# Optimization experiments

Measured on AMD Instinct MI355X. Metric: run time of the kernel, lower is better.

Reference implementation:

```python
import jax, jax.numpy as jnp
import numpy as np

# E8P 12-bit-abs codebook construction (faithful vectorized port of the torch code)
_SHUF = np.array([0, 2, 1, 3, 4, 6, 5, 7])  # shuffle_map
# get_norm12() * 2 (the integer matrix before the /2)
_NORM12_X2 = np.array([
    [3, 1, 1, 1, 3, 3, 3, 3], [1, 3, 1, 1, 3, 3, 3, 3], [1, 1, 3, 1, 3, 3, 3, 3],
    [1, 1, 1, 3, 3, 3, 3, 3], [3, 3, 3, 1, 3, 3, 1, 1], [3, 3, 3, 1, 3, 1, 3, 1],
    [3, 3, 3, 1, 1, 3, 3, 1], [3, 3, 3, 1, 3, 1, 1, 3], [3, 3, 3, 1, 1, 3, 1, 3],
    [3, 3, 3, 1, 1, 1, 3, 3], [3, 3, 1, 3, 3, 3, 1, 1], [3, 3, 1, 3, 3, 1, 3, 1],
    [3, 3, 1, 3, 1, 3, 3, 1], [3, 3, 1, 3, 3, 1, 1, 3], [3, 3, 1, 3, 1, 3, 1, 3],
    [3, 3, 1, 3, 1, 1, 3, 3], [3, 1, 3, 3, 3, 3, 1, 1], [3, 1, 3, 3, 3, 1, 3, 1],
    [3, 1, 3, 3, 1, 3, 3, 1], [3, 1, 3, 3, 3, 1, 1, 3], [3, 1, 3, 3, 1, 3, 1, 3],
    [1, 3, 3, 3, 1, 1, 3, 3], [1, 3, 3, 3, 3, 3, 1, 1], [1, 3, 3, 3, 3, 1, 3, 1],
    [1, 3, 3, 3, 1, 3, 3, 1], [1, 3, 3, 3, 3, 1, 1, 3], [1, 3, 3, 3, 1, 3, 1, 3],
    [1, 1, 3, 3, 1, 3, 3, 3], [3, 3, 1, 1, 3, 3, 3, 1]], dtype=np.int64)


def _packed_abs_grid():
    # Enumerate D8+1/2 lattice points, working with doubled integer coords (odd ints in [-7,7])
    idx = np.arange(8 ** 8, dtype=np.int64)
    cols, s, nrm = [], 0, 0
    for i in range(8):  # torch.cartesian_prod order: first dim varies slowest
        v = (2 * (((idx >> (3 * (7 - i))) & 7) - 4) + 1).astype(np.int8)  # 2*x for x in {-3.5..3.5}
        cols.append(v)
        w = v.astype(np.int32)
        s = s + w
        nrm = nrm + w * w
    mask = (s % 4 == 0) & (nrm <= 40)
    V = np.stack([c[mask] for c in cols], axis=1)
    d8abs2 = np.unique(np.abs(V), axis=0).astype(np.int64)  # lexsorted, doubled abs values
    cba2 = np.concatenate([d8abs2, _NORM12_X2], axis=0)[:, _SHUF]  # doubled values (== 2*cba)
    parity = (cba2.sum(1) // 2) % 2  # == cba.sum(1) % 2
    col = cba2 * 2  # == cba * 4, integer byte values in [2,14]
    col[:, 7] = col[:, 7] * (1 - 2 * parity)
    acc = np.zeros(col.shape[0], dtype=np.int64)
    for i in range(8):
        acc = acc | (col[:, i] << (8 * i))
    assert acc.shape[0] == 256
    return acc


def _full_grid():
    # Decode all 2^16 codes into the [65536, 8] fp32 codebook (port of get_full_grid)
    acc = _packed_abs_grid()
    c = np.arange(1 << 16, dtype=np.int64)
    signs = c & 255
    p = signs ^ (signs >> 4)
    p ^= p >> 2
    p ^= p >> 1
    parity = p & 1  # xor of the 8 sign bits
    signs = signs ^ parity
    ac = acc[c >> 8]  # packed abs code per entry
    byt = ((ac[:, None] >> (8 * _SHUF)) & 255).astype(np.uint8).astype(np.int8).astype(np.float32) / 4.0
    neg = ((signs[:, None] >> (7 - _SHUF)) & 1).astype(bool)
    vals = np.where(neg, -byt, byt) + np.where(parity[:, None] == 1, np.float32(-0.25), np.float32(0.25))
    return vals.astype(np.float32)


def setup_inputs() -> dict:
    key = jax.random.key(0)
    k1, k2 = jax.random.split(key)
    B = 4096          # tokens (batch * seq)
    M = 4096          # out_features = Qidxs rows
    N = 512           # Qidxs cols; in_features = N * 8 = 4096
    inp = jax.random.normal(k1, (B, N * 8), dtype=jnp.float32)
    Qidxs = jax.random.randint(k2, (M, N), 0, 1 << 16, dtype=jnp.int32)
    grid = jnp.asarray(_full_grid())  # [65536, 8] fp32 decoded E8P codebook
    return {"input": inp, "Qidxs": Qidxs, "grid": grid}


def reference(input, Qidxs, grid):
    m, n = Qidxs.shape
    # Dequantize: each int16 code indexes an 8-vector of the E8P codebook
    W = jnp.take(grid, Qidxs, axis=0).reshape(m, n * 8)  # [m, n*8] decompressed weight
    return input @ W.T  # [B, m]
```

## Files before the change

kernel.cpp:

```cpp
#include <hip/hip_runtime.h>
#include <hip/hip_bf16.h>

#define B_DIM 4096
#define M_DIM 4096
#define K_DIM 4096
#define NCODE 512

typedef __attribute__((ext_vector_type(4))) float f32x4;
typedef __attribute__((ext_vector_type(8))) short short8;

__device__ __forceinline__ unsigned short f2bf(float f) {
    union { float f; unsigned u; } c; c.f = f;
    unsigned u = c.u;
    return (unsigned short)((u + 0x7FFFu + ((u >> 16) & 1u)) >> 16);
}

__global__ __launch_bounds__(256) void prep_kernel(const int* __restrict__ Q,
                                                   const float* __restrict__ cb,
                                                   short* __restrict__ Wout,
                                                   const float* __restrict__ in,
                                                   short* __restrict__ Ab) {
    const int b = blockIdx.x;
    if (b < 8192) {
        const int t = b * 256 + threadIdx.x;
        const int code = Q[t] & 0xFFFF;
        const float4* g = (const float4*)(cb + (size_t)code * 8);
        const float4 v0 = g[0];
        const float4 v1 = g[1];
        short8 o;
        o[0] = f2bf(v0.x); o[1] = f2bf(v0.y); o[2] = f2bf(v0.z); o[3] = f2bf(v0.w);
        o[4] = f2bf(v1.x); o[5] = f2bf(v1.y); o[6] = f2bf(v1.z); o[7] = f2bf(v1.w);
        *(short8*)(Wout + (size_t)t * 8) = o;
    } else {
        const int t = (b - 8192) * 256 + threadIdx.x;
        const float4* p = (const float4*)(in + (size_t)t * 8);
        const float4 v0 = p[0];
        const float4 v1 = p[1];
        short8 o;
        o[0] = f2bf(v0.x); o[1] = f2bf(v0.y); o[2] = f2bf(v0.z); o[3] = f2bf(v0.w);
        o[4] = f2bf(v1.x); o[5] = f2bf(v1.y); o[6] = f2bf(v1.z); o[7] = f2bf(v1.w);
        *(short8*)(Ab + (size_t)t * 8) = o;
    }
}

#define BM 256
#define BN 256
#define BK 32
#define NT (K_DIM / BK)

#define GLD(src, dst) \
    __builtin_amdgcn_global_load_lds( \
        (const __attribute__((address_space(1))) void*)(src), \
        (__attribute__((address_space(3))) void*)(dst), 16, 0, 0)

#define MFMA(a, b, c) __builtin_amdgcn_mfma_f32_16x16x32_bf16(a, b, c, 0, 0, 0)

__global__ __launch_bounds__(512, 2) void gemm_bt_kernel(const short* __restrict__ A,
                                                         const short* __restrict__ Wd,
                                                         float* __restrict__ C) {
    __shared__ short lds[4 * 16384];

    const int tid  = threadIdx.x;
    const int wave = tid >> 6;
    const int lane = tid & 63;

    const int bid = blockIdx.x;
    const int xcd = bid & 7;
    const int s   = bid >> 3;
    const int by  = (xcd >> 1) * 4 + (s >> 3);
    const int bx  = (xcd & 1) * 8 + (s & 7);

    const int rowBase = by * BM;
    const int colBase = bx * BN;

    const int wr = wave >> 2;
    const int wc = wave & 3;

    const int rA0 = tid >> 2;
    const int uu  = (tid & 3) ^ ((rA0 >> 1) & 3);
    const short* aSrc0 = A  + (size_t)(rowBase + rA0) * K_DIM + uu * 8;
    const short* aSrc1 = A  + (size_t)(rowBase + rA0 + 128) * K_DIM + uu * 8;
    const short* bSrc0 = Wd + (size_t)(colBase + rA0) * K_DIM + uu * 8;
    const short* bSrc1 = Wd + (size_t)(colBase + rA0 + 128) * K_DIM + uu * 8;

    const int l15 = lane & 15;
    const int l4  = lane >> 4;
    const int sx  = (l15 >> 1) & 3;
    const int aRd = (wr * 128 + l15) * 32 + (l4 ^ sx) * 8;
    const int bRd = 8192 + (wc * 64 + l15) * 32 + (l4 ^ sx) * 8;

    f32x4 acc[8][4] = {};

#pragma unroll
    for (int p = 0; p < 3; ++p) {
        const int koff = p * BK;
        short* base = &lds[p * 16384];
        GLD(aSrc0 + koff, base + wave * 512);
        GLD(aSrc1 + koff, base + 4096 + wave * 512);
        GLD(bSrc0 + koff, base + 8192 + wave * 512);
        GLD(bSrc1 + koff, base + 12288 + wave * 512);
    }
    asm volatile("s_waitcnt vmcnt(8)" ::: "memory");
    __builtin_amdgcn_s_barrier();

    for (int t = 0; t < NT; ++t) {
        const int buf    = (t & 3) * 16384;
        const int tpre   = (t + 3 < NT) ? (t + 3) : (NT - 1);
        const int kpre   = tpre * BK;
        const int bufpre = ((t + 3) & 3) * 16384;

        short8 a0[4], b0[4];
#pragma unroll
        for (int m = 0; m < 4; ++m)
            a0[m] = *(const short8*)&lds[buf + aRd + m * 512];
#pragma unroll
        for (int n = 0; n < 4; ++n)
            b0[n] = *(const short8*)&lds[buf + bRd + n * 512];
        GLD(aSrc0 + kpre, &lds[bufpre + wave * 512]);
        GLD(aSrc1 + kpre, &lds[bufpre + 4096 + wave * 512]);
        asm volatile("s_waitcnt vmcnt(6)" ::: "memory");
        __builtin_amdgcn_s_barrier();
        asm volatile("s_waitcnt lgkmcnt(0)" ::: "memory");
        __builtin_amdgcn_sched_barrier(0);
        __builtin_amdgcn_s_setprio(1);
#pragma unroll
        for (int m = 0; m < 4; ++m)
#pragma unroll
            for (int n = 0; n < 4; ++n)
                acc[m][n] = MFMA(a0[m], b0[n], acc[m][n]);
        __builtin_amdgcn_s_setprio(0);
        __builtin_amdgcn_s_barrier();

        short8 a1[4];
#pragma unroll
        for (int m = 0; m < 4; ++m)
            a1[m] = *(const short8*)&lds[buf + aRd + (m + 4) * 512];
        GLD(bSrc0 + kpre, &lds[bufpre + 8192 + wave * 512]);
        GLD(bSrc1 + kpre, &lds[bufpre + 12288 + wave * 512]);
        __builtin_amdgcn_s_barrier();
        asm volatile("s_waitcnt lgkmcnt(0)" ::: "memory");
        __builtin_amdgcn_sched_barrier(0);
        __builtin_amdgcn_s_setprio(1);
#pragma unroll
        for (int m = 0; m < 4; ++m)
#pragma unroll
            for (int n = 0; n < 4; ++n)
                acc[m + 4][n] = MFMA(a1[m], b0[n], acc[m + 4][n]);
        __builtin_amdgcn_s_setprio(0);
        __builtin_amdgcn_s_barrier();
    }

    const int r0 = rowBase + wr * 128 + l4 * 4;
    const int c0 = colBase + wc * 64 + l15;
#pragma unroll
    for (int m = 0; m < 8; ++m)
#pragma unroll
        for (int n = 0; n < 4; ++n) {
            float* cp = C + (size_t)(r0 + m * 16) * M_DIM + (c0 + n * 16);
#pragma unroll
            for (int reg = 0; reg < 4; ++reg)
                cp[(size_t)reg * M_DIM] = acc[m][n][reg];
        }
}

extern "C" void kernel_launch(void* const* d_in, const int* in_sizes, int n_in,
                              void* d_out, int out_size, void* d_ws, size_t ws_size,
                              hipStream_t stream) {
    const float* inp  = (const float*)d_in[0];
    const int*   qidx = (const int*)d_in[1];
    const float* cb   = (const float*)d_in[2];
    float* out = (float*)d_out;

    short* Wb = (short*)d_ws;
    short* Ab = Wb + (size_t)M_DIM * K_DIM;

    prep_kernel<<<16384, 256, 0, stream>>>(qidx, cb, Wb, inp, Ab);

    gemm_bt_kernel<<<256, 512, 0, stream>>>(Ab, Wb, out);
}
```

Measured before the change: 147.7 us.

## Restructure GEMM main loop to BK=64 double-buffered pipeline with register prefetch

Doubles the K tile to 64 and replaces the 4-stage BK=32 LDS ring with a 2-stage double buffer. Each iteration now runs four MFMA phases, with the next tile's first fragments preloaded into registers across the barrier and a new 8-way XOR swizzle for the 64-wide rows. The aim is fewer barriers per unit of K and better overlap of LDS reads and global loads with MFMA work. The cost is less prefetch depth, since only one tile is in flight. It also waits on vmcnt(0) every iteration, which can expose global load latency, and holds more live fragment registers.

Result: faster. 133.4 us, median of 3 (-9.7%).

```diff
diff --git a/kernel.cpp b/kernel.cpp
--- a/kernel.cpp
+++ b/kernel.cpp
@@ -45,7 +45,7 @@
 
 #define BM 256
 #define BN 256
-#define BK 32
+#define BK 64
 #define NT (K_DIM / BK)
 
 #define GLD(src, dst) \
@@ -58,7 +58,7 @@
 __global__ __launch_bounds__(512, 2) void gemm_bt_kernel(const short* __restrict__ A,
                                                          const short* __restrict__ Wd,
                                                          float* __restrict__ C) {
-    __shared__ short lds[4 * 16384];
+    __shared__ short lds[2 * 32768];
 
     const int tid  = threadIdx.x;
     const int wave = tid >> 6;
@@ -76,77 +76,101 @@
     const int wr = wave >> 2;
     const int wc = wave & 3;
 
-    const int rA0 = tid >> 2;
-    const int uu  = (tid & 3) ^ ((rA0 >> 1) & 3);
-    const short* aSrc0 = A  + (size_t)(rowBase + rA0) * K_DIM + uu * 8;
-    const short* aSrc1 = A  + (size_t)(rowBase + rA0 + 128) * K_DIM + uu * 8;
-    const short* bSrc0 = Wd + (size_t)(colBase + rA0) * K_DIM + uu * 8;
-    const short* bSrc1 = Wd + (size_t)(colBase + rA0 + 128) * K_DIM + uu * 8;
+    const int rA0 = tid >> 3;
+    const int uu  = (tid & 7) ^ (rA0 & 7);
+    const int stOff = rA0 * 64 + (tid & 7) * 8;
+    const short* aSrcB = A  + (size_t)(rowBase + rA0) * K_DIM + uu * 8;
+    const short* bSrcB = Wd + (size_t)(colBase + rA0) * K_DIM + uu * 8;
 
     const int l15 = lane & 15;
     const int l4  = lane >> 4;
-    const int sx  = (l15 >> 1) & 3;
-    const int aRd = (wr * 128 + l15) * 32 + (l4 ^ sx) * 8;
-    const int bRd = 8192 + (wc * 64 + l15) * 32 + (l4 ^ sx) * 8;
+    const int uk0 = ((l4 ^ (l15 & 7))) * 8;
+    const int uk1 = uk0 ^ 32;
+    const int aRow = (wr * 128 + l15) * 64;
+    const int bRow = 16384 + (wc * 64 + l15) * 64;
 
     f32x4 acc[8][4] = {};
-
-#pragma unroll
-    for (int p = 0; p < 3; ++p) {
-        const int koff = p * BK;
-        short* base = &lds[p * 16384];
-        GLD(aSrc0 + koff, base + wave * 512);
-        GLD(aSrc1 + koff, base + 4096 + wave * 512);
-        GLD(bSrc0 + koff, base + 8192 + wave * 512);
-        GLD(bSrc1 + koff, base + 12288 + wave * 512);
-    }
-    asm volatile("s_waitcnt vmcnt(8)" ::: "memory");
+    short8 aC[4], bC[4];
+
+#pragma unroll
+    for (int c = 0; c < 4; ++c)
+        GLD(aSrcB + c * (64 * K_DIM), &lds[c * 4096 + stOff]);
+#pragma unroll
+    for (int c = 0; c < 4; ++c)
+        GLD(bSrcB + c * (64 * K_DIM), &lds[16384 + c * 4096 + stOff]);
+    asm volatile("s_waitcnt vmcnt(0)" ::: "memory");
     __builtin_amdgcn_s_barrier();
+#pragma unroll
+    for (int m = 0; m < 4; ++m) aC[m] = *(const short8*)&lds[aRow + m * 1024 + uk0];
+#pragma unroll
+    for (int n = 0; n < 4; ++n) bC[n] = *(const short8*)&lds[bRow + n * 1024 + uk0];
 
     for (int t = 0; t < NT; ++t) {
-        const int buf    = (t & 3) * 16384;
-        const int tpre   = (t + 3 < NT) ? (t + 3) : (NT - 1);
-        const int kpre   = tpre * BK;
-        const int bufpre = ((t + 3) & 3) * 16384;
-
-        short8 a0[4], b0[4];
-#pragma unroll
-        for (int m = 0; m < 4; ++m)
-            a0[m] = *(const short8*)&lds[buf + aRd + m * 512];
+        const int buf  = (t & 1) * 32768;
+        const int bufn = buf ^ 32768;
+        const size_t kpre = (size_t)(((t + 1 < NT) ? (t + 1) : (NT - 1)) * BK);
+
+        short8 a1h0[4];
+#pragma unroll
+        for (int m = 0; m < 4; ++m)
+            a1h0[m] = *(const short8*)&lds[buf + aRow + (m + 4) * 1024 + uk0];
+#pragma unroll
+        for (int c = 0; c < 4; ++c)
+            GLD(aSrcB + kpre + c * (64 * K_DIM), &lds[bufn + c * 4096 + stOff]);
+        __builtin_amdgcn_s_setprio(1);
+#pragma unroll
+        for (int m = 0; m < 4; ++m)
+#pragma unroll
+            for (int n = 0; n < 4; ++n)
+                acc[m][n] = MFMA(aC[m], bC[n], acc[m][n]);
+        __builtin_amdgcn_s_setprio(0);
+
+        short8 a0h1[4], b1[4];
+#pragma unroll
+        for (int m = 0; m < 4; ++m)
+            a0h1[m] = *(const short8*)&lds[buf + aRow + m * 1024 + uk1];
 #pragma unroll
         for (int n = 0; n < 4; ++n)
-            b0[n] = *(const short8*)&lds[buf + bRd + n * 512];
-        GLD(aSrc0 + kpre, &lds[bufpre + wave * 512]);
-        GLD(aSrc1 + kpre, &lds[bufpre + 4096 + wave * 512]);
-        asm volatile("s_waitcnt vmcnt(6)" ::: "memory");
+            b1[n] = *(const short8*)&lds[buf + bRow + n * 1024 + uk1];
+#pragma unroll
+        for (int c = 0; c < 4; ++c)
+            GLD(bSrcB + kpre + c * (64 * K_DIM), &lds[bufn + 16384 + c * 4096 + stOff]);
+        __builtin_amdgcn_s_setprio(1);
+#pragma unroll
+        for (int m = 0; m < 4; ++m)
+#pragma unroll
+            for (int n = 0; n < 4; ++n)
+                acc[m + 4][n] = MFMA(a1h0[m], bC[n], acc[m + 4][n]);
+        __builtin_amdgcn_s_setprio(0);
+
+        short8 a1h1[4];
+#pragma unroll
+        for (int m = 0; m < 4; ++m)
+            a1h1[m] = *(const short8*)&lds[buf + aRow + (m + 4) * 1024 + uk1];
+        __builtin_amdgcn_s_setprio(1);
+#pragma unroll
+        for (int m = 0; m < 4; ++m)
+#pragma unroll
+            for (int n = 0; n < 4; ++n)
+                acc[m][n] = MFMA(a0h1[m], b1[n], acc[m][n]);
+        __builtin_amdgcn_s_setprio(0);
+        asm volatile("s_waitcnt vmcnt(0)" ::: "memory");
         __builtin_amdgcn_s_barrier();
-        asm volatile("s_waitcnt lgkmcnt(0)" ::: "memory");
-        __builtin_amdgcn_sched_barrier(0);
-        __builtin_amdgcn_s_setprio(1);
-#pragma unroll
-        for (int m = 0; m < 4; ++m)
-#pragma unroll
-            for (int n = 0; n < 4; ++n)
-                acc[m][n] = MFMA(a0[m], b0[n], acc[m][n]);
-        __builtin_amdgcn_s_setprio(0);
-        __builtin_amdgcn_s_barrier();
-
-        short8 a1[4];
-#pragma unroll
-        for (int m = 0; m < 4; ++m)
-            a1[m] = *(const short8*)&lds[buf + aRd + (m + 4) * 512];
-        GLD(bSrc0 + kpre, &lds[bufpre + 8192 + wave * 512]);
-        GLD(bSrc1 + kpre, &lds[bufpre + 12288 + wave * 512]);
-        __builtin_amdgcn_s_barrier();
-        asm volatile("s_waitcnt lgkmcnt(0)" ::: "memory");
-        __builtin_amdgcn_sched_barrier(0);
-        __builtin_amdgcn_s_setprio(1);
-#pragma unroll
-        for (int m = 0; m < 4; ++m)
-#pragma unroll
-            for (int n = 0; n < 4; ++n)
-                acc[m + 4][n] = MFMA(a1[m], b0[n], acc[m + 4][n]);
-        __builtin_amdgcn_s_setprio(0);
+
+#pragma unroll
+        for (int m = 0; m < 4; ++m)
+            aC[m] = *(const short8*)&lds[bufn + aRow + m * 1024 + uk0];
+#pragma unroll
+        for (int n = 0; n < 4; ++n)
+            bC[n] = *(const short8*)&lds[bufn + bRow + n * 1024 + uk0];
+        __builtin_amdgcn_s_setprio(1);
+#pragma unroll
+        for (int m = 0; m < 4; ++m)
+#pragma unroll
+            for (int n = 0; n < 4; ++n)
+                acc[m + 4][n] = MFMA(a1h1[m], b1[n], acc[m + 4][n]);
+        __builtin_amdgcn_s_setprio(0);
+        asm volatile("s_waitcnt lgkmcnt(8)" ::: "memory");
         __builtin_amdgcn_s_barrier();
     }
 
```

## Shrink GEMM tile to 256x128 with 4 waves and triple-buffered prefetch pipeline

Applied to the files above, without the earlier changes.

Changes the GEMM block tile from 256x256 with 8 waves to 256x128 with 4 waves, launching 512 blocks instead of 256. It replaces the 4-stage LDS ring with a 3-buffer ring prefetching two tiles ahead. Next-tile fragments are loaded into registers after a single barrier per iteration instead of four, and the LDS swizzle pattern changes. The aim is lower barrier and synchronisation overhead and more blocks per CU, at the cost of less data reuse per tile and more global traffic for A.

After: 160.0 us. 8.3% more time.

```diff
diff --git a/kernel.cpp b/kernel.cpp
--- a/kernel.cpp
+++ b/kernel.cpp
@@ -44,9 +44,10 @@
 }
 
 #define BM 256
-#define BN 256
+#define BN 128
 #define BK 32
 #define NT (K_DIM / BK)
+#define BUFS 12288
 
 #define GLD(src, dst) \
     __builtin_amdgcn_global_load_lds( \
@@ -55,10 +56,10 @@
 
 #define MFMA(a, b, c) __builtin_amdgcn_mfma_f32_16x16x32_bf16(a, b, c, 0, 0, 0)
 
-__global__ __launch_bounds__(512, 2) void gemm_bt_kernel(const short* __restrict__ A,
+__global__ __launch_bounds__(256, 2) void gemm_bt_kernel(const short* __restrict__ A,
                                                          const short* __restrict__ Wd,
                                                          float* __restrict__ C) {
-    __shared__ short lds[4 * 16384];
+    __shared__ short lds[3 * BUFS];
 
     const int tid  = threadIdx.x;
     const int wave = tid >> 6;
@@ -67,87 +68,87 @@
     const int bid = blockIdx.x;
     const int xcd = bid & 7;
     const int s   = bid >> 3;
-    const int by  = (xcd >> 1) * 4 + (s >> 3);
-    const int bx  = (xcd & 1) * 8 + (s & 7);
+    const int by  = (xcd >> 1) * 4 + (s >> 4);
+    const int bx  = (xcd & 1) * 16 + (s & 15);
 
     const int rowBase = by * BM;
     const int colBase = bx * BN;
 
-    const int wr = wave >> 2;
-    const int wc = wave & 3;
+    const int wr = wave >> 1;
+    const int wc = wave & 1;
 
     const int rA0 = tid >> 2;
-    const int uu  = (tid & 3) ^ ((rA0 >> 1) & 3);
-    const short* aSrc0 = A  + (size_t)(rowBase + rA0) * K_DIM + uu * 8;
-    const short* aSrc1 = A  + (size_t)(rowBase + rA0 + 128) * K_DIM + uu * 8;
-    const short* bSrc0 = Wd + (size_t)(colBase + rA0) * K_DIM + uu * 8;
-    const short* bSrc1 = Wd + (size_t)(colBase + rA0 + 128) * K_DIM + uu * 8;
+    const int uu  = (tid & 3) ^ (rA0 & 3);
+    const int stOff = rA0 * 32 + (tid & 3) * 8;
+    const short* aSrcB = A  + (size_t)(rowBase + rA0) * K_DIM + uu * 8;
+    const short* bSrcB = Wd + (size_t)(colBase + rA0) * K_DIM + uu * 8;
+
+#define STAGE(tt, base) { \
+        const size_t ko = (size_t)(tt) * BK; \
+        GLD(aSrcB + ko,                 &lds[(base) + stOff]); \
+        GLD(aSrcB + ko + 1 * 64 * K_DIM, &lds[(base) + 2048 + stOff]); \
+        GLD(aSrcB + ko + 2 * 64 * K_DIM, &lds[(base) + 4096 + stOff]); \
+        GLD(aSrcB + ko + 3 * 64 * K_DIM, &lds[(base) + 6144 + stOff]); \
+        GLD(bSrcB + ko,                 &lds[(base) + 8192 + stOff]); \
+        GLD(bSrcB + ko + 1 * 64 * K_DIM, &lds[(base) + 8192 + 2048 + stOff]); }
 
     const int l15 = lane & 15;
     const int l4  = lane >> 4;
-    const int sx  = (l15 >> 1) & 3;
+    const int sx  = l15 & 3;
     const int aRd = (wr * 128 + l15) * 32 + (l4 ^ sx) * 8;
     const int bRd = 8192 + (wc * 64 + l15) * 32 + (l4 ^ sx) * 8;
 
     f32x4 acc[8][4] = {};
+    short8 aC[4], bC[4];
 
+    STAGE(0, 0);
+    STAGE(1, BUFS);
+    asm volatile("s_waitcnt vmcnt(6)" ::: "memory");
+    __builtin_amdgcn_s_barrier();
 #pragma unroll
-    for (int p = 0; p < 3; ++p) {
-        const int koff = p * BK;
-        short* base = &lds[p * 16384];
-        GLD(aSrc0 + koff, base + wave * 512);
-        GLD(aSrc1 + koff, base + 4096 + wave * 512);
-        GLD(bSrc0 + koff, base + 8192 + wave * 512);
-        GLD(bSrc1 + koff, base + 12288 + wave * 512);
-    }
-    asm volatile("s_waitcnt vmcnt(8)" ::: "memory");
-    __builtin_amdgcn_s_barrier();
+    for (int m = 0; m < 4; ++m) aC[m] = *(const short8*)&lds[aRd + m * 512];
+#pragma unroll
+    for (int n = 0; n < 4; ++n) bC[n] = *(const short8*)&lds[bRd + n * 512];
 
+    int bi = 0;
     for (int t = 0; t < NT; ++t) {
-        const int buf    = (t & 3) * 16384;
-        const int tpre   = (t + 3 < NT) ? (t + 3) : (NT - 1);
-        const int kpre   = tpre * BK;
-        const int bufpre = ((t + 3) & 3) * 16384;
+        const int cur  = bi * BUFS;
+        const int bn1i = (bi + 1 < 3) ? (bi + 1) : 0;
+        const int bn2i = (bn1i + 1 < 3) ? (bn1i + 1) : 0;
+        const int bn1  = bn1i * BUFS;
+        const int bn2  = bn2i * BUFS;
+        const int t2c  = (t + 2 < NT) ? (t + 2) : (NT - 1);
 
-        short8 a0[4], b0[4];
+        short8 a1[4];
 #pragma unroll
         for (int m = 0; m < 4; ++m)
-            a0[m] = *(const short8*)&lds[buf + aRd + m * 512];
-#pragma unroll
-        for (int n = 0; n < 4; ++n)
-            b0[n] = *(const short8*)&lds[buf + bRd + n * 512];
-        GLD(aSrc0 + kpre, &lds[bufpre + wave * 512]);
-        GLD(aSrc1 + kpre, &lds[bufpre + 4096 + wave * 512]);
-        asm volatile("s_waitcnt vmcnt(6)" ::: "memory");
-        __builtin_amdgcn_s_barrier();
-        asm volatile("s_waitcnt lgkmcnt(0)" ::: "memory");
-        __builtin_amdgcn_sched_barrier(0);
+            a1[m] = *(const short8*)&lds[cur + aRd + (m + 4) * 512];
+        STAGE(t2c, bn2);
         __builtin_amdgcn_s_setprio(1);
 #pragma unroll
         for (int m = 0; m < 4; ++m)
 #pragma unroll
             for (int n = 0; n < 4; ++n)
-                acc[m][n] = MFMA(a0[m], b0[n], acc[m][n]);
+                acc[m][n] = MFMA(aC[m], bC[n], acc[m][n]);
         __builtin_amdgcn_s_setprio(0);
-        __builtin_amdgcn_s_barrier();
 
-        short8 a1[4];
-#pragma unroll
-        for (int m = 0; m < 4; ++m)
-            a1[m] = *(const short8*)&lds[buf + aRd + (m + 4) * 512];
-        GLD(bSrc0 + kpre, &lds[bufpre + 8192 + wave * 512]);
-        GLD(bSrc1 + kpre, &lds[bufpre + 12288 + wave * 512]);
-        __builtin_amdgcn_s_barrier();
-        asm volatile("s_waitcnt lgkmcnt(0)" ::: "memory");
-        __builtin_amdgcn_sched_barrier(0);
         __builtin_amdgcn_s_setprio(1);
 #pragma unroll
         for (int m = 0; m < 4; ++m)
 #pragma unroll
             for (int n = 0; n < 4; ++n)
-                acc[m + 4][n] = MFMA(a1[m], b0[n], acc[m + 4][n]);
+                acc[m + 4][n] = MFMA(a1[m], bC[n], acc[m + 4][n]);
         __builtin_amdgcn_s_setprio(0);
+        asm volatile("s_waitcnt vmcnt(6)" ::: "memory");
         __builtin_amdgcn_s_barrier();
+#pragma unroll
+        for (int m = 0; m < 4; ++m)
+            aC[m] = *(const short8*)&lds[bn1 + aRd + m * 512];
+#pragma unroll
+        for (int n = 0; n < 4; ++n)
+            bC[n] = *(const short8*)&lds[bn1 + bRd + n * 512];
+
+        bi = bn1i;
     }
 
     const int r0 = rowBase + wr * 128 + l4 * 4;
@@ -176,5 +177,5 @@
 
     prep_kernel<<<16384, 256, 0, stream>>>(qidx, cb, Wb, inp, Ab);
 
-    gemm_bt_kernel<<<256, 512, 0, stream>>>(Ab, Wb, out);
+    gemm_bt_kernel<<<512, 256, 0, stream>>>(Ab, Wb, out);
 }
```
